# Kernel optimization log

Measured on AMD Instinct MI355X. Metric: run time of the kernel, lower is better.

## Reference

```python
import jax, jax.numpy as jnp
import numpy as np

B, S, DIM = 2, 2048, 2048
N_HEADS, N_KV_HEADS = 32, 8
HEAD_DIM = DIM // N_HEADS  # 64
N_REP = N_HEADS // N_KV_HEADS  # 4
ROPE_THETA = 10000.0


def setup_inputs() -> dict:
    key = jax.random.key(0)
    ks = jax.random.split(key, 5)
    x = jax.random.normal(ks[0], (B, S, DIM), dtype=jnp.float32)
    # rope frequencies: freqs_cis[t, j] = exp(i * t * theta^(-2j/head_dim))
    inv_freq = 1.0 / (ROPE_THETA ** (jnp.arange(0, HEAD_DIM, 2, dtype=jnp.float32) / HEAD_DIM))
    angles = jnp.arange(S, dtype=jnp.float32)[:, None] * inv_freq[None, :]  # [S, HEAD_DIM//2]
    freqs_cos = jnp.cos(angles)
    freqs_sin = jnp.sin(angles)
    scale = 1.0 / np.sqrt(DIM)
    wq = jax.random.normal(ks[1], (N_HEADS * HEAD_DIM, DIM), dtype=jnp.float32) * scale
    wk = jax.random.normal(ks[2], (N_KV_HEADS * HEAD_DIM, DIM), dtype=jnp.float32) * scale
    wv = jax.random.normal(ks[3], (N_KV_HEADS * HEAD_DIM, DIM), dtype=jnp.float32) * scale
    wo = jax.random.normal(ks[4], (DIM, N_HEADS * HEAD_DIM), dtype=jnp.float32) * scale
    return {"x": x, "freqs_cos": freqs_cos, "freqs_sin": freqs_sin,
            "wq": wq, "wk": wk, "wv": wv, "wo": wo}


def _rope(t, cos, sin):
    # t: [B, S, H, D]; rotate consecutive pairs (even, odd) lanes -- complex mul.
    t = t.reshape(*t.shape[:-1], HEAD_DIM // 2, 2)
    t0, t1 = t[..., 0], t[..., 1]
    c = cos[None, :, None, :]  # [1, S, 1, D//2]
    s = sin[None, :, None, :]
    r0 = t0 * c - t1 * s
    r1 = t0 * s + t1 * c
    return jnp.stack([r0, r1], axis=-1).reshape(*t0.shape[:-1], HEAD_DIM)


def reference(x, freqs_cos, freqs_sin, wq, wk, wv, wo):
    bsz, seqlen, _ = x.shape
    xq = jnp.einsum('bsd,hd->bsh', x, wq).reshape(bsz, seqlen, N_HEADS, HEAD_DIM)
    xk = jnp.einsum('bsd,hd->bsh', x, wk).reshape(bsz, seqlen, N_KV_HEADS, HEAD_DIM)
    xv = jnp.einsum('bsd,hd->bsh', x, wv).reshape(bsz, seqlen, N_KV_HEADS, HEAD_DIM)
    xq = _rope(xq, freqs_cos[:seqlen], freqs_sin[:seqlen])
    xk = _rope(xk, freqs_cos[:seqlen], freqs_sin[:seqlen])
    # GQA: repeat_interleave kv heads to n_heads
    xk = jnp.repeat(xk, N_REP, axis=2)
    xv = jnp.repeat(xv, N_REP, axis=2)
    # [B, H, S, D]
    q = xq.transpose(0, 2, 1, 3)
    k = xk.transpose(0, 2, 1, 3)
    v = xv.transpose(0, 2, 1, 3)
    scores = jnp.einsum('bhqd,bhkd->bhqk', q, k) / np.sqrt(HEAD_DIM)
    causal = jnp.tril(jnp.ones((seqlen, seqlen), dtype=bool))
    scores = jnp.where(causal[None, None], scores, jnp.finfo(scores.dtype).min)
    attn = jax.nn.softmax(scores, axis=-1)
    out = jnp.einsum('bhqk,bhkd->bhqd', attn, v)
    out = out.transpose(0, 2, 1, 3).reshape(bsz, seqlen, N_HEADS * HEAD_DIM)
    return jnp.einsum('bsh,dh->bsd', out, wo)
```

## Files before the change

kernel.cpp:

```cpp
#include <hip/hip_runtime.h>
#include <hip/hip_bf16.h>
#include <stdint.h>

#define BATCH 2
#define SEQ   2048
#define DIM   2048
#define NH    32
#define NKV   8
#define HD    64
#define QKVN  3072
#define MROWS 4096

typedef __bf16 bf16x8 __attribute__((ext_vector_type(8)));
typedef float  f32x4  __attribute__((ext_vector_type(4)));
typedef unsigned short ushort8v __attribute__((ext_vector_type(8)));

typedef __attribute__((address_space(3))) void lds_void;
typedef const __attribute__((address_space(1))) void gbl_void;

__device__ __forceinline__ void gload_lds16(const void* g, void* l) {
    __builtin_amdgcn_global_load_lds((gbl_void*)g, (lds_void*)l, 16, 0, 0);
}

__global__ void cvt_f32_bf16(const float* __restrict__ in,
                             __hip_bfloat16* __restrict__ out, int n) {
    int i = (blockIdx.x * 256 + threadIdx.x) * 4;
    if (i >= n) return;
    const float4 v = *reinterpret_cast<const float4*>(in + i);
    union { ushort4 u; __hip_bfloat16 h[4]; } o;
    o.h[0] = __float2bfloat16(v.x);
    o.h[1] = __float2bfloat16(v.y);
    o.h[2] = __float2bfloat16(v.z);
    o.h[3] = __float2bfloat16(v.w);
    *reinterpret_cast<ushort4*>(out + i) = o.u;
}

__device__ __forceinline__ void store_out(float* p, float v) { *p = v; }
__device__ __forceinline__ void store_out(__hip_bfloat16* p, float v) { *p = __float2bfloat16(v); }

template <typename OUT_T>
__global__ __launch_bounds__(256) void gemm_bt(
    const __hip_bfloat16* __restrict__ A,
    const __hip_bfloat16* __restrict__ B,
    OUT_T* __restrict__ C,
    int M, int N, int K)
{
    __shared__ __align__(16) __hip_bfloat16 As[128 * 32];
    __shared__ __align__(16) __hip_bfloat16 Bs[128 * 32];
    const int tid  = threadIdx.x;
    const int lane = tid & 63;
    const int wave = tid >> 6;
    const int wr = wave >> 1, wc = wave & 1;
    const int lr = lane & 15, lg = lane >> 4;
    const size_t tm = (size_t)blockIdx.x * 128;
    const size_t tn = (size_t)blockIdx.y * 128;

    f32x4 acc[4][4] = {};

    const int srow  = tid >> 2;
    const int scol  = (tid & 3) * 8;
    const int wbase = wave * 512;

    const __hip_bfloat16* pa = As + (wr * 64 + lr) * 32 + lg * 8;
    const __hip_bfloat16* pb = Bs + (wc * 64 + lr) * 32 + lg * 8;

    for (int k0 = 0; k0 < K; k0 += 32) {
        const __hip_bfloat16* gA = A + (tm + srow) * (size_t)K + k0 + scol;
        const __hip_bfloat16* gB = B + (tn + srow) * (size_t)K + k0 + scol;
        gload_lds16(gA,                 (void*)(As + wbase));
        gload_lds16(gA + (size_t)64*K,  (void*)(As + 2048 + wbase));
        gload_lds16(gB,                 (void*)(Bs + wbase));
        gload_lds16(gB + (size_t)64*K,  (void*)(Bs + 2048 + wbase));
        __syncthreads();
        bf16x8 af[4], bfr[4];
        #pragma unroll
        for (int m = 0; m < 4; ++m) af[m]  = *reinterpret_cast<const bf16x8*>(pa + m * 512);
        #pragma unroll
        for (int n = 0; n < 4; ++n) bfr[n] = *reinterpret_cast<const bf16x8*>(pb + n * 512);
        #pragma unroll
        for (int m = 0; m < 4; ++m)
            #pragma unroll
            for (int n = 0; n < 4; ++n)
                acc[m][n] = __builtin_amdgcn_mfma_f32_16x16x32_bf16(af[m], bfr[n], acc[m][n], 0, 0, 0);
        __syncthreads();
    }

    #pragma unroll
    for (int m = 0; m < 4; ++m)
        #pragma unroll
        for (int n = 0; n < 4; ++n)
            #pragma unroll
            for (int r = 0; r < 4; ++r) {
                size_t row = tm + wr * 64 + m * 16 + lg * 4 + r;
                size_t col = tn + wc * 64 + n * 16 + lr;
                store_out(&C[row * (size_t)N + col], acc[m][n][r]);
            }
}

__global__ void rope_qk(const __hip_bfloat16* __restrict__ qkv,
                        const float* __restrict__ fcos,
                        const float* __restrict__ fsin,
                        __hip_bfloat16* __restrict__ outp,
                        int nheads, int col_off, float mul) {
    int idx = blockIdx.x * 256 + threadIdx.x;
    int i  = idx & 31;
    int s  = (idx >> 5) & (SEQ - 1);
    int bh = idx >> 16;
    int h  = bh % nheads;
    const __hip_bfloat16* src = qkv + ((size_t)(bh / nheads) * SEQ + s) * QKVN
                                    + col_off + h * HD + 2 * i;
    union { unsigned int u; __hip_bfloat16 h2[2]; } in_, out_;
    in_.u = *reinterpret_cast<const unsigned int*>(src);
    float t0 = __bfloat162float(in_.h2[0]);
    float t1 = __bfloat162float(in_.h2[1]);
    float c  = fcos[s * 32 + i] * mul;
    float sn = fsin[s * 32 + i] * mul;
    out_.h2[0] = __float2bfloat16(t0 * c - t1 * sn);
    out_.h2[1] = __float2bfloat16(t0 * sn + t1 * c);
    *reinterpret_cast<unsigned int*>(outp + ((size_t)bh * SEQ + s) * HD + 2 * i) = out_.u;
}

__global__ __launch_bounds__(256) void v_repack(const __hip_bfloat16* __restrict__ qkv,
                                                __hip_bfloat16* __restrict__ vt) {
    __shared__ unsigned short tile[64][66];
    int blk = blockIdx.x;
    int st = blk & 31;
    int kh = (blk >> 5) & 7;
    int b  = blk >> 8;
    int s0 = st * 64;
    int t  = threadIdx.x;
    int r  = t >> 2;
    #pragma unroll
    for (int it = 0; it < 2; ++it) {
        int chunk = (t & 3) + it * 4;
        const __hip_bfloat16* src = qkv + ((size_t)(b * SEQ + s0 + r)) * QKVN
                                        + 2560 + kh * HD + chunk * 8;
        ushort8v v = *reinterpret_cast<const ushort8v*>(src);
        #pragma unroll
        for (int j = 0; j < 8; ++j) tile[r][chunk * 8 + j] = v[j];
    }
    __syncthreads();
    int d = t >> 2;
    #pragma unroll
    for (int it = 0; it < 2; ++it) {
        int chunk = (t & 3) + it * 4;
        ushort8v w;
        #pragma unroll
        for (int j = 0; j < 8; ++j) w[j] = tile[chunk * 8 + j][d];
        *reinterpret_cast<ushort8v*>(vt + ((size_t)(b * NKV + kh) * HD + d) * SEQ
                                        + s0 + chunk * 8) = w;
    }
}

__device__ __forceinline__ unsigned pack_bf16x2(float lo, float hi) {
    __hip_bfloat162 t;
    t.x = __float2bfloat16(lo);
    t.y = __float2bfloat16(hi);
    return *reinterpret_cast<unsigned*>(&t);
}

__global__ __launch_bounds__(256, 4) void flash_attn(
    const __hip_bfloat16* __restrict__ Qp,
    const __hip_bfloat16* __restrict__ Kp,
    const __hip_bfloat16* __restrict__ Vt,
    __hip_bfloat16* __restrict__ O) {
    __shared__ __align__(16) __hip_bfloat16 Kst[2][4096];
    __shared__ __align__(16) __hip_bfloat16 Vst[2][4096];
    __shared__ __align__(16) unsigned char Plds[4][2048];
    const int qt   = (int)gridDim.x - 1 - (int)blockIdx.x;
    const int bh   = blockIdx.y;
    const int b    = bh >> 5, h = bh & 31;
    const int kvh  = h >> 2;
    const int tid  = threadIdx.x;
    const int wave = tid >> 6, lane = tid & 63;
    const int lr = lane & 15, lg = lane >> 4;
    const int qw0 = qt * 64 + wave * 16;

    const __hip_bfloat16* qbase = Qp + (((size_t)bh) * SEQ + qw0 + lr) * HD + lg * 8;
    const bf16x8 qa0 = *reinterpret_cast<const bf16x8*>(qbase);
    const bf16x8 qa1 = *reinterpret_cast<const bf16x8*>(qbase + 32);

    const __hip_bfloat16* kb = Kp + ((size_t)(b * NKV + kvh) * SEQ) * HD;
    const __hip_bfloat16* vb = Vt + ((size_t)(b * NKV + kvh) * HD) * SEQ;

    const int srow = tid >> 3;
    const int sch  = (tid & 7) ^ (srow & 7);
    const size_t koff0 = (size_t)srow        * HD  + sch * 8;
    const size_t koff1 = (size_t)(srow + 32) * HD  + sch * 8;
    const size_t voff0 = (size_t)srow        * SEQ + sch * 8;
    const size_t voff1 = (size_t)(srow + 32) * SEQ + sch * 8;
    const int wvb = wave * 1024;

    int foff[4][2];
    #pragma unroll
    for (int g = 0; g < 4; ++g)
        #pragma unroll
        for (int c = 0; c < 2; ++c)
            foff[g][c] = (g * 16 + lr) * 64 + (((c * 4 + lg) ^ (lr & 7)) * 8);

    f32x4 acc[4] = {};
    float m_run = -1e30f, l_run = 0.f;

    unsigned char* pw = &Plds[wave][0];
    const int swz = (lr & 7) << 4;
    const int kv_end = qt * 64 + 64;

    {
        char* kd = (char*)&Kst[0][0];
        char* vd = (char*)&Vst[0][0];
        gload_lds16(kb + koff0, kd + wvb);
        gload_lds16(kb + koff1, kd + 4096 + wvb);
        gload_lds16(vb + voff0, vd + wvb);
        gload_lds16(vb + voff1, vd + 4096 + wvb);
    }
    int cur = 0;

    for (int kv0 = 0; kv0 < kv_end; kv0 += 64) {
        __syncthreads();
        if (kv0 + 64 < kv_end) {
            const __hip_bfloat16* ks = kb + (size_t)(kv0 + 64) * HD;
            const __hip_bfloat16* vs = vb + (kv0 + 64);
            char* kd = (char*)&Kst[cur ^ 1][0];
            char* vd = (char*)&Vst[cur ^ 1][0];
            gload_lds16(ks + koff0, kd + wvb);
            gload_lds16(ks + koff1, kd + 4096 + wvb);
            gload_lds16(vs + voff0, vd + wvb);
            gload_lds16(vs + voff1, vd + 4096 + wvb);
        }
        const __hip_bfloat16* Kl = &Kst[cur][0];
        const __hip_bfloat16* Vl = &Vst[cur][0];

        f32x4 s[4];
        #pragma unroll
        for (int nk = 0; nk < 4; ++nk) {
            bf16x8 k0 = *reinterpret_cast<const bf16x8*>(Kl + foff[nk][0]);
            bf16x8 k1 = *reinterpret_cast<const bf16x8*>(Kl + foff[nk][1]);
            f32x4 z = {0.f, 0.f, 0.f, 0.f};
            z = __builtin_amdgcn_mfma_f32_16x16x32_bf16(k0, qa0, z, 0, 0, 0);
            z = __builtin_amdgcn_mfma_f32_16x16x32_bf16(k1, qa1, z, 0, 0, 0);
            s[nk] = z;
        }
        if (kv0 + 64 >= kv_end) {
            const int qg = qw0 + lr;
            #pragma unroll
            for (int nk = 0; nk < 4; ++nk) {
                const int kbase = kv0 + nk * 16 + lg * 4;
                #pragma unroll
                for (int r = 0; r < 4; ++r)
                    if (kbase + r > qg) s[nk][r] = -1e30f;
            }
        }
        float tmax = fmaxf(fmaxf(s[0][0], s[0][1]), fmaxf(s[0][2], s[0][3]));
        #pragma unroll
        for (int nk = 1; nk < 4; ++nk)
            tmax = fmaxf(tmax, fmaxf(fmaxf(s[nk][0], s[nk][1]), fmaxf(s[nk][2], s[nk][3])));
        tmax = fmaxf(tmax, __shfl_xor(tmax, 16, 64));
        tmax = fmaxf(tmax, __shfl_xor(tmax, 32, 64));
        const float mn    = fmaxf(m_run, tmax);
        const float alpha = __expf(m_run - mn);
        m_run = mn;
        float tsum = 0.f;
        #pragma unroll
        for (int nk = 0; nk < 4; ++nk) {
            float p0 = __expf(s[nk][0] - m_run);
            float p1 = __expf(s[nk][1] - m_run);
            float p2 = __expf(s[nk][2] - m_run);
            float p3 = __expf(s[nk][3] - m_run);
            tsum += (p0 + p1) + (p2 + p3);
            uint2 pk;
            pk.x = pack_bf16x2(p0, p1);
            pk.y = pack_bf16x2(p2, p3);
            *reinterpret_cast<uint2*>(pw + lr * 128 + ((nk * 32 + lg * 8) ^ swz)) = pk;
        }
        tsum += __shfl_xor(tsum, 16, 64);
        tsum += __shfl_xor(tsum, 32, 64);
        l_run = l_run * alpha + tsum;
        float a0 = __shfl(alpha, lg * 4 + 0, 64);
        float a1 = __shfl(alpha, lg * 4 + 1, 64);
        float a2 = __shfl(alpha, lg * 4 + 2, 64);
        float a3 = __shfl(alpha, lg * 4 + 3, 64);
        #pragma unroll
        for (int nd = 0; nd < 4; ++nd) {
            acc[nd][0] *= a0; acc[nd][1] *= a1;
            acc[nd][2] *= a2; acc[nd][3] *= a3;
        }
        asm volatile("s_waitcnt lgkmcnt(0)" ::: "memory");
        __builtin_amdgcn_sched_barrier(0);
        const bf16x8 pa0 = *reinterpret_cast<const bf16x8*>(pw + lr * 128 + ((     lg * 16) ^ swz));
        const bf16x8 pa1 = *reinterpret_cast<const bf16x8*>(pw + lr * 128 + ((64 + lg * 16) ^ swz));
        #pragma unroll
        for (int nd = 0; nd < 4; ++nd) {
            bf16x8 v0 = *reinterpret_cast<const bf16x8*>(Vl + foff[nd][0]);
            bf16x8 v1 = *reinterpret_cast<const bf16x8*>(Vl + foff[nd][1]);
            acc[nd] = __builtin_amdgcn_mfma_f32_16x16x32_bf16(pa0, v0, acc[nd], 0, 0, 0);
            acc[nd] = __builtin_amdgcn_mfma_f32_16x16x32_bf16(pa1, v1, acc[nd], 0, 0, 0);
        }
        cur ^= 1;
    }
    float linv[4];
    #pragma unroll
    for (int r = 0; r < 4; ++r)
        linv[r] = 1.f / __shfl(l_run, lg * 4 + r, 64);
    #pragma unroll
    for (int nd = 0; nd < 4; ++nd)
        #pragma unroll
        for (int r = 0; r < 4; ++r) {
            int qg  = qw0 + lg * 4 + r;
            int col = h * HD + nd * 16 + lr;
            O[((size_t)(b * SEQ + qg)) * DIM + col] = __float2bfloat16(acc[nd][r] * linv[r]);
        }
}

extern "C" void kernel_launch(void* const* d_in, const int* in_sizes, int n_in,
                              void* d_out, int out_size, void* d_ws, size_t ws_size,
                              hipStream_t stream) {
    const float* x    = (const float*)d_in[0];
    const float* fcos = (const float*)d_in[1];
    const float* fsin = (const float*)d_in[2];
    const float* wq   = (const float*)d_in[3];
    const float* wk   = (const float*)d_in[4];
    const float* wv   = (const float*)d_in[5];
    const float* wo   = (const float*)d_in[6];
    float* out = (float*)d_out;

    __hip_bfloat16* Xb   = (__hip_bfloat16*)d_ws;
    __hip_bfloat16* Wqkv = Xb   + (size_t)MROWS * DIM;
    __hip_bfloat16* Wob  = Wqkv + (size_t)QKVN * DIM;
    __hip_bfloat16* QKV  = Wob  + (size_t)DIM * DIM;
    __hip_bfloat16* Qp   = QKV  + (size_t)MROWS * QKVN;
    __hip_bfloat16* Kp   = Qp   + (size_t)BATCH * NH * SEQ * HD;
    __hip_bfloat16* Vt   = Kp   + (size_t)BATCH * NKV * SEQ * HD;
    __hip_bfloat16* AO   = Xb;

    cvt_f32_bf16<<<(MROWS * DIM) / 1024, 256, 0, stream>>>(x, Xb, MROWS * DIM);
    cvt_f32_bf16<<<(DIM * DIM) / 1024, 256, 0, stream>>>(wq, Wqkv, DIM * DIM);
    cvt_f32_bf16<<<(NKV * HD * DIM) / 1024, 256, 0, stream>>>(wk, Wqkv + (size_t)DIM * DIM, NKV * HD * DIM);
    cvt_f32_bf16<<<(NKV * HD * DIM) / 1024, 256, 0, stream>>>(wv, Wqkv + (size_t)(DIM + NKV * HD) * DIM, NKV * HD * DIM);
    cvt_f32_bf16<<<(DIM * DIM) / 1024, 256, 0, stream>>>(wo, Wob, DIM * DIM);

    gemm_bt<__hip_bfloat16><<<dim3(MROWS / 128, QKVN / 128), 256, 0, stream>>>(
        Xb, Wqkv, QKV, MROWS, QKVN, DIM);

    rope_qk<<<(BATCH * NH * SEQ * 32) / 256, 256, 0, stream>>>(QKV, fcos, fsin, Qp, NH, 0, 0.125f);
    rope_qk<<<(BATCH * NKV * SEQ * 32) / 256, 256, 0, stream>>>(QKV, fcos, fsin, Kp, NKV, DIM, 1.0f);
    v_repack<<<BATCH * NKV * 32, 256, 0, stream>>>(QKV, Vt);

    flash_attn<<<dim3(SEQ / 64, BATCH * NH), 256, 0, stream>>>(Qp, Kp, Vt, AO);

    gemm_bt<float><<<dim3(MROWS / 128, DIM / 128), 256, 0, stream>>>(
        AO, Wob, out, MROWS, DIM, DIM);
}
```

Baseline: 386.6 us.

## Add lazy softmax rescaling and XCD-aware block remapping in GEMM

```diff
diff --git a/kernel.cpp b/kernel.cpp
--- a/kernel.cpp
+++ b/kernel.cpp
@@ -52,8 +52,13 @@
     const int wave = tid >> 6;
     const int wr = wave >> 1, wc = wave & 1;
     const int lr = lane & 15, lg = lane >> 4;
-    const size_t tm = (size_t)blockIdx.x * 128;
-    const size_t tn = (size_t)blockIdx.y * 128;
+
+    const int nwg = (int)(gridDim.x * gridDim.y);
+    const int id  = (int)blockIdx.y * (int)gridDim.x + (int)blockIdx.x;
+    const int cpx = nwg >> 3;
+    const int sw  = (id & 7) * cpx + (id >> 3);
+    const size_t tm = (size_t)(sw % (int)gridDim.x) * 128;
+    const size_t tn = (size_t)(sw / (int)gridDim.x) * 128;
 
     f32x4 acc[4][4] = {};
 
@@ -199,7 +204,8 @@
             foff[g][c] = (g * 16 + lr) * 64 + (((c * 4 + lg) ^ (lr & 7)) * 8);
 
     f32x4 acc[4] = {};
-    float m_run = -1e30f, l_run = 0.f;
+    float m_run = -1e30f;
+    float l_run = 0.f;
 
     unsigned char* pw = &Plds[wave][0];
     const int swz = (lr & 7) << 4;
@@ -250,15 +256,27 @@
                     if (kbase + r > qg) s[nk][r] = -1e30f;
             }
         }
-        float tmax = fmaxf(fmaxf(s[0][0], s[0][1]), fmaxf(s[0][2], s[0][3]));
+        float pmax = fmaxf(fmaxf(s[0][0], s[0][1]), fmaxf(s[0][2], s[0][3]));
         #pragma unroll
         for (int nk = 1; nk < 4; ++nk)
-            tmax = fmaxf(tmax, fmaxf(fmaxf(s[nk][0], s[nk][1]), fmaxf(s[nk][2], s[nk][3])));
-        tmax = fmaxf(tmax, __shfl_xor(tmax, 16, 64));
-        tmax = fmaxf(tmax, __shfl_xor(tmax, 32, 64));
-        const float mn    = fmaxf(m_run, tmax);
-        const float alpha = __expf(m_run - mn);
-        m_run = mn;
+            pmax = fmaxf(pmax, fmaxf(fmaxf(s[nk][0], s[nk][1]), fmaxf(s[nk][2], s[nk][3])));
+        if (!__all(pmax - m_run <= 8.0f)) {
+            float tmax = fmaxf(pmax, __shfl_xor(pmax, 16, 64));
+            tmax = fmaxf(tmax, __shfl_xor(tmax, 32, 64));
+            const float mn    = fmaxf(m_run, tmax);
+            const float alpha = __expf(m_run - mn);
+            m_run = mn;
+            l_run *= alpha;
+            const float a0 = __shfl(alpha, lg * 4 + 0, 64);
+            const float a1 = __shfl(alpha, lg * 4 + 1, 64);
+            const float a2 = __shfl(alpha, lg * 4 + 2, 64);
+            const float a3 = __shfl(alpha, lg * 4 + 3, 64);
+            #pragma unroll
+            for (int nd = 0; nd < 4; ++nd) {
+                acc[nd][0] *= a0; acc[nd][1] *= a1;
+                acc[nd][2] *= a2; acc[nd][3] *= a3;
+            }
+        }
         float tsum = 0.f;
         #pragma unroll
         for (int nk = 0; nk < 4; ++nk) {
@@ -272,18 +290,7 @@
             pk.y = pack_bf16x2(p2, p3);
             *reinterpret_cast<uint2*>(pw + lr * 128 + ((nk * 32 + lg * 8) ^ swz)) = pk;
         }
-        tsum += __shfl_xor(tsum, 16, 64);
-        tsum += __shfl_xor(tsum, 32, 64);
-        l_run = l_run * alpha + tsum;
-        float a0 = __shfl(alpha, lg * 4 + 0, 64);
-        float a1 = __shfl(alpha, lg * 4 + 1, 64);
-        float a2 = __shfl(alpha, lg * 4 + 2, 64);
-        float a3 = __shfl(alpha, lg * 4 + 3, 64);
-        #pragma unroll
-        for (int nd = 0; nd < 4; ++nd) {
-            acc[nd][0] *= a0; acc[nd][1] *= a1;
-            acc[nd][2] *= a2; acc[nd][3] *= a3;
-        }
+        l_run += tsum;
         asm volatile("s_waitcnt lgkmcnt(0)" ::: "memory");
         __builtin_amdgcn_sched_barrier(0);
         const bf16x8 pa0 = *reinterpret_cast<const bf16x8*>(pw + lr * 128 + ((     lg * 16) ^ swz));
@@ -297,10 +304,13 @@
         }
         cur ^= 1;
     }
+    float lt = l_run;
+    lt += __shfl_xor(lt, 16, 64);
+    lt += __shfl_xor(lt, 32, 64);
     float linv[4];
     #pragma unroll
     for (int r = 0; r < 4; ++r)
-        linv[r] = 1.f / __shfl(l_run, lg * 4 + r, 64);
+        linv[r] = 1.f / __shfl(lt, lg * 4 + r, 64);
     #pragma unroll
     for (int nd = 0; nd < 4; ++nd)
         #pragma unroll
```

Result: faster. 371.5 us (-3.9%).
